# Kernel tuning notes

Hardware: AMD Instinct MI355X
Metric: run time of the kernel (lower is better)

## Reference

```python
import jax, jax.numpy as jnp
import numpy as np

E = 65536
MUL0, MUL1 = 32, 16              # multiplicities of 0e and 1o in irreps_in1/out
FC_IN, FC_HID = 64, 64
WNUMEL = MUL0*MUL0 + MUL1*MUL0 + MUL0*MUL1 + MUL1*MUL1  # 2304
SILU_NORM = 1.6790                # e3nn normalize2mom constant for silu
ISQRT3 = float(1.0 / np.sqrt(3.0))  # w3j entries for l<=1 paths


def setup_inputs() -> dict:
    key = jax.random.key(0)
    k1, k2, k3, k4, k5 = jax.random.split(key, 5)
    return {
        "fea_in1": jax.random.normal(k1, (E, MUL0 + 3 * MUL1), jnp.float32),
        "fea_in2": jax.random.normal(k2, (E, 4), jnp.float32),
        "fea_weight": jax.random.normal(k3, (E, FC_IN), jnp.float32),
        "W1": jax.random.normal(k4, (FC_IN, FC_HID), jnp.float32),
        "W2": jax.random.normal(k5, (FC_HID, WNUMEL), jnp.float32),
    }


def reference(fea_in1, fea_in2, fea_weight, W1, W2):
    # --- e3nn FullyConnectedNet: variance-preserving linear + normalized silu ---
    h = SILU_NORM * jax.nn.silu(fea_weight @ (W1 / np.sqrt(FC_IN)))   # [E, FC_HID]
    w = h @ (W2 / np.sqrt(FC_HID))                                    # [E, WNUMEL]

    # --- split generated per-edge weights into the 4 uvw paths ---
    s0 = MUL0 * MUL0
    s1 = s0 + MUL1 * MUL0
    s2 = s1 + MUL0 * MUL1
    w00 = w[:, :s0].reshape(E, MUL0, MUL0)     # 0e x 0e -> 0e
    w110 = w[:, s0:s1].reshape(E, MUL1, MUL0)  # 1o x 1o -> 0e
    w011 = w[:, s1:s2].reshape(E, MUL0, MUL1)  # 0e x 1o -> 1o
    w101 = w[:, s2:].reshape(E, MUL1, MUL1)    # 1o x 0e -> 1o

    # --- split irrep blocks ---
    x1_0 = fea_in1[:, :MUL0]                       # [E, 32]
    x1_1 = fea_in1[:, MUL0:].reshape(E, MUL1, 3)   # [E, 16, 3]
    x2_0 = fea_in2[:, 0]                           # [E]
    x2_1 = fea_in2[:, 1:4]                         # [E, 3]

    # path weights: sqrt(ir_out.dim / (mul_in1*mul_in2 * n_paths_to_output))
    pw00 = float(np.sqrt(1.0 / (MUL0 * 2)))
    pw110 = float(np.sqrt(1.0 / (MUL1 * 2)))
    pw011 = float(np.sqrt(3.0 / (MUL0 * 2)))
    pw101 = float(np.sqrt(3.0 / (MUL1 * 2)))

    # CG contractions (w3j(0,0,0)=1, w3j(1,1,0)=delta/sqrt3, w3j(0,1,1)=w3j(1,0,1)=delta/sqrt3)
    out0 = pw00 * jnp.einsum('eu,e,euw->ew', x1_0, x2_0, w00) \
         + (pw110 * ISQRT3) * jnp.einsum('eui,ei,euw->ew', x1_1, x2_1, w110)   # [E, 32]
    out1 = (pw011 * ISQRT3) * jnp.einsum('eu,ek,euw->ewk', x1_0, x2_1, w011) \
         + (pw101 * ISQRT3) * jnp.einsum('eui,e,euw->ewi', x1_1, x2_0, w101)   # [E, 16, 3]

    return jnp.concatenate([out0, out1.reshape(E, 3 * MUL1)], axis=1)          # [E, 80]
```

## Files before the change

kernel.cpp:

```cpp
#include <hip/hip_runtime.h>
#include <hip/hip_bf16.h>

typedef __attribute__((ext_vector_type(8)))  __bf16 bf16x8;
typedef __attribute__((ext_vector_type(16))) float  f32x16;

#define N_TILES   72
#define W2F_ELEMS (72*4*64*8)
#define W1F_ELEMS (2*4*64*8)

__global__ __launch_bounds__(256) void equiconv_prep(const float* __restrict__ W1,
                                                     const float* __restrict__ W2,
                                                     __bf16* __restrict__ W1F,
                                                     __bf16* __restrict__ W2F) {
    int idx = blockIdx.x * 256 + threadIdx.x;
    if (idx < W2F_ELEMS) {
        int j  = idx & 7;
        int ln = (idx >> 3) & 63;
        int ks = (idx >> 9) & 3;
        int t  = idx >> 11;
        int m  = 32 * t + (ln & 31);
        int c  = ks * 16 + 8 * (ln >> 5) + j;
        W2F[idx] = (__bf16)(W2[c * 2304 + m] * 0.125f);
    } else {
        int i2 = idx - W2F_ELEMS;
        if (i2 < W1F_ELEMS) {
            int j  = i2 & 7;
            int ln = (i2 >> 3) & 63;
            int ks = (i2 >> 9) & 3;
            int mt = i2 >> 11;
            int c  = 32 * mt + (ln & 31);
            int in = ks * 16 + 8 * (ln >> 5) + j;
            W1F[i2] = (__bf16)(W1[in * 64 + c] * 0.125f);
        }
    }
}

#define X10f(u, el)    smemf[(u)*128 + (el)]
#define CB1f(u, el)    smemf[4096 + (u)*128 + (el)]
#define X11f(k, u, el) smemf[6144 + ((k)*16 + (u))*128 + (el)]
#define F2f(el, j)     smemf[12288 + (el)*4 + (j)]

__global__ __launch_bounds__(256) void equiconv_main(const float* __restrict__ fea_in1,
                                                     const float* __restrict__ fea_in2,
                                                     const float* __restrict__ fea_w,
                                                     const __bf16* __restrict__ W2F,
                                                     const __bf16* __restrict__ W1F,
                                                     float* __restrict__ out) {
    __shared__ __align__(16) float smemf[16896];
    __bf16* HT = (__bf16*)(smemf + 12800);

    const int tid  = threadIdx.x;
    const int lane = tid & 63;
    const int wv   = tid >> 6;
    const int l31  = lane & 31;
    const int hi   = lane >> 5;
    const int eBlk = blockIdx.x * 128;
    const int eLoc = wv * 32 + l31;
    const int sw   = (eLoc & 7) << 3;

    for (int i = tid; i < 128 * 80; i += 256) {
        float v = fea_in1[(size_t)eBlk * 80 + i];
        int el = i / 80;
        int j  = i - el * 80;
        if (j < 32) {
            X10f(j, el) = v;
        } else {
            int jj = j - 32;
            int u  = jj / 3;
            int k  = jj - u * 3;
            X11f(k, u, el) = v;
        }
    }
    for (int i = tid; i < 128 * 4; i += 256)
        F2f(i >> 2, i & 3) = fea_in2[(size_t)eBlk * 4 + i];
    __syncthreads();

    const float c110 = 0.10206207261596577f;
    for (int i = tid; i < 16 * 128; i += 256) {
        int u = i >> 7, el = i & 127;
        CB1f(u, el) = c110 * (X11f(0, u, el) * F2f(el, 1) +
                              X11f(1, u, el) * F2f(el, 2) +
                              X11f(2, u, el) * F2f(el, 3));
    }

    const f32x16 Z16 = {0,0,0,0,0,0,0,0,0,0,0,0,0,0,0,0};
    {
        bf16x8 bw[4];
        const float* pw = fea_w + (size_t)(eBlk + eLoc) * 64 + hi * 8;
#pragma unroll
        for (int ks = 0; ks < 4; ++ks) {
            float4 u0 = *(const float4*)(pw + ks * 16);
            float4 u1 = *(const float4*)(pw + ks * 16 + 4);
            bf16x8 b;
            b[0] = (__bf16)u0.x; b[1] = (__bf16)u0.y; b[2] = (__bf16)u0.z; b[3] = (__bf16)u0.w;
            b[4] = (__bf16)u1.x; b[5] = (__bf16)u1.y; b[6] = (__bf16)u1.z; b[7] = (__bf16)u1.w;
            bw[ks] = b;
        }
        f32x16 h0 = Z16, h1 = Z16;
#pragma unroll
        for (int ks = 0; ks < 4; ++ks) {
            bf16x8 a0 = *(const bf16x8*)(W1F + (size_t)((0 * 4 + ks) * 64 + lane) * 8);
            h0 = __builtin_amdgcn_mfma_f32_32x32x16_bf16(a0, bw[ks], h0, 0, 0, 0);
            bf16x8 a1 = *(const bf16x8*)(W1F + (size_t)((1 * 4 + ks) * 64 + lane) * 8);
            h1 = __builtin_amdgcn_mfma_f32_32x32x16_bf16(a1, bw[ks], h1, 0, 0, 0);
        }
#pragma unroll
        for (int r = 0; r < 16; ++r) {
            int rv = (r & 3) + 8 * (r >> 2) + 4 * hi;
            float x0 = h0[r];
            HT[eLoc * 64 + (rv ^ sw)]        = (__bf16)(1.679f * x0 / (1.f + expf(-x0)));
            float x1 = h1[r];
            HT[eLoc * 64 + ((32 + rv) ^ sw)] = (__bf16)(1.679f * x1 / (1.f + expf(-x1)));
        }
    }
    __syncthreads();

    const float x20  = F2f(eLoc, 0);
    const float x21a = F2f(eLoc, 1), x21b = F2f(eLoc, 2), x21c = F2f(eLoc, 3);
    const float sA0  = 0.125f * x20;
    const float s101 = 0.17677669529663687f * x20;

    bf16x8 hfr[4];
#pragma unroll
    for (int ks = 0; ks < 4; ++ks)
        hfr[ks] = *(const bf16x8*)&HT[eLoc * 64 + ((ks * 16 + 8 * hi) ^ sw)];

    float acc0[16];
    float t011[8];
    float t101[3][8];
#pragma unroll
    for (int r = 0; r < 16; ++r) acc0[r] = 0.f;
#pragma unroll
    for (int s = 0; s < 8; ++s) { t011[s] = 0.f; t101[0][s] = 0.f; t101[1][s] = 0.f; t101[2][s] = 0.f; }

    const __bf16* const pW2l = W2F + (size_t)lane * 8;

#define LOADA(dst, T) {                                                   \
        dst[0] = *(const bf16x8*)(pW2l + (size_t)((T) * 4 + 0) * 512);    \
        dst[1] = *(const bf16x8*)(pW2l + (size_t)((T) * 4 + 1) * 512);    \
        dst[2] = *(const bf16x8*)(pW2l + (size_t)((T) * 4 + 2) * 512);    \
        dst[3] = *(const bf16x8*)(pW2l + (size_t)((T) * 4 + 3) * 512); }

#define MFMA_T(Cv, Af) {                                                          \
        Cv = __builtin_amdgcn_mfma_f32_32x32x16_bf16(Af[0], hfr[0], Z16, 0,0,0);  \
        Cv = __builtin_amdgcn_mfma_f32_32x32x16_bf16(Af[1], hfr[1], Cv,  0,0,0);  \
        Cv = __builtin_amdgcn_mfma_f32_32x32x16_bf16(Af[2], hfr[2], Cv,  0,0,0);  \
        Cv = __builtin_amdgcn_mfma_f32_32x32x16_bf16(Af[3], hfr[3], Cv,  0,0,0); }

#define EPI_W00(TT) { float cf = sA0 * X10f((TT), eLoc);                          \
        _Pragma("unroll") for (int r = 0; r < 16; ++r) acc0[r] += cf * Cv[r]; }
#define EPI_W110(TT) { float cf = CB1f((TT) - 32, eLoc);                          \
        _Pragma("unroll") for (int r = 0; r < 16; ++r) acc0[r] += cf * Cv[r]; }
#define EPI_W011(TT) { int uu = 2 * ((TT) - 48);                                  \
        float cf0 = X10f(uu, eLoc), cf1 = X10f(uu + 1, eLoc);                     \
        _Pragma("unroll") for (int r = 0; r < 16; ++r)                            \
            t011[r & 7] += (r >= 8 ? cf1 : cf0) * Cv[r]; }
#define EPI_W101(TT) { int uu = 2 * ((TT) - 64);                                  \
        float d00 = X11f(0, uu, eLoc), d01 = X11f(1, uu, eLoc), d02 = X11f(2, uu, eLoc);          \
        float d10 = X11f(0, uu + 1, eLoc), d11 = X11f(1, uu + 1, eLoc), d12 = X11f(2, uu + 1, eLoc); \
        _Pragma("unroll") for (int r = 0; r < 16; ++r) {                          \
            int s = r & 7;                                                        \
            t101[0][s] += (r >= 8 ? d10 : d00) * Cv[r];                           \
            t101[1][s] += (r >= 8 ? d11 : d01) * Cv[r];                           \
            t101[2][s] += (r >= 8 ? d12 : d02) * Cv[r]; } }

#define RUN_PHASE(BASE, NT, NEXTT, LAST, EPI)                                     \
    _Pragma("unroll")                                                             \
    for (int t = 0; t < (NT); ++t) {                                              \
        const int cur = (BASE) + t;                                               \
        const int nxt = (t + 1 < (NT)) ? (cur + 1) : (NEXTT);                     \
        f32x16 Cv;                                                                \
        if ((t & 1) == 0) {                                                       \
            if (!(LAST) || (t + 1 < (NT))) LOADA(aQ, nxt);                        \
            MFMA_T(Cv, aP);                                                       \
        } else {                                                                  \
            if (!(LAST) || (t + 1 < (NT))) LOADA(aP, nxt);                        \
            MFMA_T(Cv, aQ);                                                       \
        }                                                                         \
        EPI(cur);                                                                 \
    }

    bf16x8 aP[4], aQ[4];
    LOADA(aP, 0);
    RUN_PHASE(0,  32, 32, false, EPI_W00)
    RUN_PHASE(32, 16, 48, false, EPI_W110)
    RUN_PHASE(48, 16, 64, false, EPI_W011)
    RUN_PHASE(64, 8,  71, true,  EPI_W101)

    __syncthreads();
    float* OST = smemf;
#pragma unroll
    for (int r = 0; r < 16; ++r) {
        int rv = (r & 3) + 8 * (r >> 2) + 4 * hi;
        OST[eLoc * 80 + rv] = acc0[r];
    }
#pragma unroll
    for (int s = 0; s < 8; ++s) {
        int w = (s & 3) + 8 * (s >> 2) + 4 * hi;
        float b011 = 0.125f * t011[s];
        OST[eLoc * 80 + 32 + w * 3 + 0] = x21a * b011 + s101 * t101[0][s];
        OST[eLoc * 80 + 32 + w * 3 + 1] = x21b * b011 + s101 * t101[1][s];
        OST[eLoc * 80 + 32 + w * 3 + 2] = x21c * b011 + s101 * t101[2][s];
    }
    __syncthreads();
    {
        float4* og = (float4*)(out + (size_t)blockIdx.x * 10240);
        const float4* os = (const float4*)smemf;
        for (int i = tid; i < 2560; i += 256) og[i] = os[i];
    }
}

extern "C" void kernel_launch(void* const* d_in, const int* in_sizes, int n_in,
                              void* d_out, int out_size, void* d_ws, size_t ws_size,
                              hipStream_t stream) {
    const float* fea_in1 = (const float*)d_in[0];
    const float* fea_in2 = (const float*)d_in[1];
    const float* fea_w   = (const float*)d_in[2];
    const float* W1      = (const float*)d_in[3];
    const float* W2      = (const float*)d_in[4];
    __bf16* W2F = (__bf16*)d_ws;
    __bf16* W1F = (__bf16*)((char*)d_ws + (size_t)W2F_ELEMS * 2);

    equiconv_prep<<<(W2F_ELEMS + W1F_ELEMS + 255) / 256, 256, 0, stream>>>(W1, W2, W1F, W2F);
    equiconv_main<<<65536 / 128, 256, 0, stream>>>(fea_in1, fea_in2, fea_w, W2F, W1F, (float*)d_out);
}
```

Measured before the change: 133.9 us.

## Stage W2 tiles into LDS via async global_load_lds double buffering

Replaces per-wave register prefetch of W2 fragments with block-cooperative global_load_lds staging into a double-buffered LDS region, adding a block barrier after each of the 72 tiles. It also builds the hidden-activation MFMA operands in registers using packed bf16 conversion and cross-lane shuffles instead of an LDS round trip, switches to fast __expf, and pads the LDS layouts (stride 129/81) to avoid bank conflicts. The goal is to cut redundant per-wave global loads of W2 and LDS traffic, but the per-tile __syncthreads and the scalar un-vectorised output stores may add stalls.

```diff
diff --git a/kernel.cpp b/kernel.cpp
--- a/kernel.cpp
+++ b/kernel.cpp
@@ -7,6 +7,18 @@
 #define N_TILES   72
 #define W2F_ELEMS (72*4*64*8)
 #define W1F_ELEMS (2*4*64*8)
+
+__device__ __forceinline__ void gload_lds16(const void* g, void* l) {
+    __builtin_amdgcn_global_load_lds(
+        (const __attribute__((address_space(1))) unsigned int*)g,
+        (__attribute__((address_space(3))) unsigned int*)l, 16, 0, 0);
+}
+
+__device__ __forceinline__ unsigned pk_bf16(float a, float b) {
+    unsigned r;
+    asm("v_cvt_pk_bf16_f32 %0, %1, %2" : "=v"(r) : "v"(a), "v"(b));
+    return r;
+}
 
 __global__ __launch_bounds__(256) void equiconv_prep(const float* __restrict__ W1,
                                                      const float* __restrict__ W2,
@@ -35,10 +47,11 @@
     }
 }
 
-#define X10f(u, el)    smemf[(u)*128 + (el)]
-#define CB1f(u, el)    smemf[4096 + (u)*128 + (el)]
-#define X11f(k, u, el) smemf[6144 + ((k)*16 + (u))*128 + (el)]
-#define F2f(el, j)     smemf[12288 + (el)*4 + (j)]
+#define X10f(u, el)    smemf[(u)*129 + (el)]
+#define CB1f(u, el)    smemf[4128 + (u)*129 + (el)]
+#define X11f(k, u, el) smemf[6192 + ((u)*3 + (k))*129 + (el)]
+#define F2f(el, j)     smemf[12384 + (el)*4 + (j)]
+#define ASTG_BASE 12896
 
 __global__ __launch_bounds__(256) void equiconv_main(const float* __restrict__ fea_in1,
                                                      const float* __restrict__ fea_in2,
@@ -46,8 +59,7 @@
                                                      const __bf16* __restrict__ W2F,
                                                      const __bf16* __restrict__ W1F,
                                                      float* __restrict__ out) {
-    __shared__ __align__(16) float smemf[16896];
-    __bf16* HT = (__bf16*)(smemf + 12800);
+    __shared__ __align__(16) float smemf[14944];
 
     const int tid  = threadIdx.x;
     const int lane = tid & 63;
@@ -56,7 +68,6 @@
     const int hi   = lane >> 5;
     const int eBlk = blockIdx.x * 128;
     const int eLoc = wv * 32 + l31;
-    const int sw   = (eLoc & 7) << 3;
 
     for (int i = tid; i < 128 * 80; i += 256) {
         float v = fea_in1[(size_t)eBlk * 80 + i];
@@ -84,6 +95,7 @@
     }
 
     const f32x16 Z16 = {0,0,0,0,0,0,0,0,0,0,0,0,0,0,0,0};
+    bf16x8 hfr0, hfr1, hfr2, hfr3;
     {
         bf16x8 bw[4];
         const float* pw = fea_w + (size_t)(eBlk + eLoc) * 64 + hi * 8;
@@ -104,27 +116,46 @@
             bf16x8 a1 = *(const bf16x8*)(W1F + (size_t)((1 * 4 + ks) * 64 + lane) * 8);
             h1 = __builtin_amdgcn_mfma_f32_32x32x16_bf16(a1, bw[ks], h1, 0, 0, 0);
         }
+        float sv[32];
 #pragma unroll
         for (int r = 0; r < 16; ++r) {
-            int rv = (r & 3) + 8 * (r >> 2) + 4 * hi;
             float x0 = h0[r];
-            HT[eLoc * 64 + (rv ^ sw)]        = (__bf16)(1.679f * x0 / (1.f + expf(-x0)));
+            sv[r]      = 1.679f * x0 / (1.f + __expf(-x0));
             float x1 = h1[r];
-            HT[eLoc * 64 + ((32 + rv) ^ sw)] = (__bf16)(1.679f * x1 / (1.f + expf(-x1)));
-        }
-    }
-    __syncthreads();
+            sv[16 + r] = 1.679f * x1 / (1.f + __expf(-x1));
+        }
+        uint4 fr[4];
+#pragma unroll
+        for (int ks = 0; ks < 4; ++ks) {
+            const int vb = 8 * ks;
+            float oa = hi ? sv[vb + 4] : sv[vb + 0];
+            float ob = hi ? sv[vb + 5] : sv[vb + 1];
+            float oc = hi ? sv[vb + 6] : sv[vb + 2];
+            float od = hi ? sv[vb + 7] : sv[vb + 3];
+            float sa = hi ? sv[vb + 0] : sv[vb + 4];
+            float sb = hi ? sv[vb + 1] : sv[vb + 5];
+            float sc = hi ? sv[vb + 2] : sv[vb + 6];
+            float sd = hi ? sv[vb + 3] : sv[vb + 7];
+            unsigned o0 = pk_bf16(oa, ob), o1 = pk_bf16(oc, od);
+            unsigned s0 = pk_bf16(sa, sb), s1 = pk_bf16(sc, sd);
+            unsigned r0 = (unsigned)__shfl_xor((int)s0, 32, 64);
+            unsigned r1 = (unsigned)__shfl_xor((int)s1, 32, 64);
+            fr[ks].x = hi ? r0 : o0;
+            fr[ks].y = hi ? r1 : o1;
+            fr[ks].z = hi ? o0 : r0;
+            fr[ks].w = hi ? o1 : r1;
+        }
+        hfr0 = *(bf16x8*)&fr[0];
+        hfr1 = *(bf16x8*)&fr[1];
+        hfr2 = *(bf16x8*)&fr[2];
+        hfr3 = *(bf16x8*)&fr[3];
+    }
 
     const float x20  = F2f(eLoc, 0);
     const float x21a = F2f(eLoc, 1), x21b = F2f(eLoc, 2), x21c = F2f(eLoc, 3);
     const float sA0  = 0.125f * x20;
     const float s101 = 0.17677669529663687f * x20;
 
-    bf16x8 hfr[4];
-#pragma unroll
-    for (int ks = 0; ks < 4; ++ks)
-        hfr[ks] = *(const bf16x8*)&HT[eLoc * 64 + ((ks * 16 + 8 * hi) ^ sw)];
-
     float acc0[16];
     float t011[8];
     float t101[3][8];
@@ -133,19 +164,14 @@
 #pragma unroll
     for (int s = 0; s < 8; ++s) { t011[s] = 0.f; t101[0][s] = 0.f; t101[1][s] = 0.f; t101[2][s] = 0.f; }
 
-    const __bf16* const pW2l = W2F + (size_t)lane * 8;
-
-#define LOADA(dst, T) {                                                   \
-        dst[0] = *(const bf16x8*)(pW2l + (size_t)((T) * 4 + 0) * 512);    \
-        dst[1] = *(const bf16x8*)(pW2l + (size_t)((T) * 4 + 1) * 512);    \
-        dst[2] = *(const bf16x8*)(pW2l + (size_t)((T) * 4 + 2) * 512);    \
-        dst[3] = *(const bf16x8*)(pW2l + (size_t)((T) * 4 + 3) * 512); }
-
-#define MFMA_T(Cv, Af) {                                                          \
-        Cv = __builtin_amdgcn_mfma_f32_32x32x16_bf16(Af[0], hfr[0], Z16, 0,0,0);  \
-        Cv = __builtin_amdgcn_mfma_f32_32x32x16_bf16(Af[1], hfr[1], Cv,  0,0,0);  \
-        Cv = __builtin_amdgcn_mfma_f32_32x32x16_bf16(Af[2], hfr[2], Cv,  0,0,0);  \
-        Cv = __builtin_amdgcn_mfma_f32_32x32x16_bf16(Af[3], hfr[3], Cv,  0,0,0); }
+    const __bf16* ASTG = (const __bf16*)(smemf + ASTG_BASE);
+    char* stgb = (char*)(smemf + ASTG_BASE);
+    const char* w2b = (const char*)W2F;
+
+#define STAGE(T, BUF) {                                                           \
+        const char* _s = w2b + ((size_t)(T) << 12) + wv * 1024 + (lane << 4);     \
+        char* _d = stgb + ((BUF) << 12) + wv * 1024;                              \
+        gload_lds16(_s, _d); }
 
 #define EPI_W00(TT) { float cf = sA0 * X10f((TT), eLoc);                          \
         _Pragma("unroll") for (int r = 0; r < 16; ++r) acc0[r] += cf * Cv[r]; }
@@ -158,55 +184,62 @@
 #define EPI_W101(TT) { int uu = 2 * ((TT) - 64);                                  \
         float d00 = X11f(0, uu, eLoc), d01 = X11f(1, uu, eLoc), d02 = X11f(2, uu, eLoc);          \
         float d10 = X11f(0, uu + 1, eLoc), d11 = X11f(1, uu + 1, eLoc), d12 = X11f(2, uu + 1, eLoc); \
-        _Pragma("unroll") for (int r = 0; r < 16; ++r) {                          \
-            int s = r & 7;                                                        \
+        _Pragma("unroll") for (int r = 0; r < 16; ++r) { int s = r & 7;           \
             t101[0][s] += (r >= 8 ? d10 : d00) * Cv[r];                           \
             t101[1][s] += (r >= 8 ? d11 : d01) * Cv[r];                           \
             t101[2][s] += (r >= 8 ? d12 : d02) * Cv[r]; } }
 
-#define RUN_PHASE(BASE, NT, NEXTT, LAST, EPI)                                     \
-    _Pragma("unroll")                                                             \
-    for (int t = 0; t < (NT); ++t) {                                              \
-        const int cur = (BASE) + t;                                               \
-        const int nxt = (t + 1 < (NT)) ? (cur + 1) : (NEXTT);                     \
+#define TILE_STEP(T, EPI) {                                                       \
+        if ((T) + 1 < N_TILES) STAGE((T) + 1, bufx ^ 1);                          \
+        const __bf16* tb = ASTG + (bufx << 11) + (lane << 3);                     \
+        bf16x8 a0 = *(const bf16x8*)(tb);                                         \
+        bf16x8 a1 = *(const bf16x8*)(tb + 512);                                   \
+        bf16x8 a2 = *(const bf16x8*)(tb + 1024);                                  \
+        bf16x8 a3 = *(const bf16x8*)(tb + 1536);                                  \
         f32x16 Cv;                                                                \
-        if ((t & 1) == 0) {                                                       \
-            if (!(LAST) || (t + 1 < (NT))) LOADA(aQ, nxt);                        \
-            MFMA_T(Cv, aP);                                                       \
-        } else {                                                                  \
-            if (!(LAST) || (t + 1 < (NT))) LOADA(aP, nxt);                        \
-            MFMA_T(Cv, aQ);                                                       \
-        }                                                                         \
-        EPI(cur);                                                                 \
-    }
-
-    bf16x8 aP[4], aQ[4];
-    LOADA(aP, 0);
-    RUN_PHASE(0,  32, 32, false, EPI_W00)
-    RUN_PHASE(32, 16, 48, false, EPI_W110)
-    RUN_PHASE(48, 16, 64, false, EPI_W011)
-    RUN_PHASE(64, 8,  71, true,  EPI_W101)
-
+        Cv = __builtin_amdgcn_mfma_f32_32x32x16_bf16(a0, hfr0, Z16, 0, 0, 0);     \
+        Cv = __builtin_amdgcn_mfma_f32_32x32x16_bf16(a1, hfr1, Cv, 0, 0, 0);      \
+        Cv = __builtin_amdgcn_mfma_f32_32x32x16_bf16(a2, hfr2, Cv, 0, 0, 0);      \
+        Cv = __builtin_amdgcn_mfma_f32_32x32x16_bf16(a3, hfr3, Cv, 0, 0, 0);      \
+        EPI(T);                                                                   \
+        __syncthreads();                                                          \
+        bufx ^= 1; }
+
+    int bufx = 0;
+    STAGE(0, 0);
     __syncthreads();
+
+#pragma unroll 2
+    for (int t = 0; t < 32; ++t) TILE_STEP(t, EPI_W00)
+#pragma unroll 2
+    for (int t = 32; t < 48; ++t) TILE_STEP(t, EPI_W110)
+#pragma unroll 2
+    for (int t = 48; t < 64; ++t) TILE_STEP(t, EPI_W011)
+#pragma unroll 2
+    for (int t = 64; t < 72; ++t) TILE_STEP(t, EPI_W101)
+
     float* OST = smemf;
 #pragma unroll
     for (int r = 0; r < 16; ++r) {
         int rv = (r & 3) + 8 * (r >> 2) + 4 * hi;
-        OST[eLoc * 80 + rv] = acc0[r];
+        OST[eLoc * 81 + rv] = acc0[r];
     }
 #pragma unroll
     for (int s = 0; s < 8; ++s) {
         int w = (s & 3) + 8 * (s >> 2) + 4 * hi;
         float b011 = 0.125f * t011[s];
-        OST[eLoc * 80 + 32 + w * 3 + 0] = x21a * b011 + s101 * t101[0][s];
-        OST[eLoc * 80 + 32 + w * 3 + 1] = x21b * b011 + s101 * t101[1][s];
-        OST[eLoc * 80 + 32 + w * 3 + 2] = x21c * b011 + s101 * t101[2][s];
+        OST[eLoc * 81 + 32 + w * 3 + 0] = x21a * b011 + s101 * t101[0][s];
+        OST[eLoc * 81 + 32 + w * 3 + 1] = x21b * b011 + s101 * t101[1][s];
+        OST[eLoc * 81 + 32 + w * 3 + 2] = x21c * b011 + s101 * t101[2][s];
     }
     __syncthreads();
     {
-        float4* og = (float4*)(out + (size_t)blockIdx.x * 10240);
-        const float4* os = (const float4*)smemf;
-        for (int i = tid; i < 2560; i += 256) og[i] = os[i];
+        float* og = out + (size_t)blockIdx.x * 10240;
+        for (int i = tid; i < 10240; i += 256) {
+            int el = i / 80;
+            int j  = i - el * 80;
+            og[i] = OST[el * 81 + j];
+        }
     }
 }
 
```

Result: faster. 123.8 us (-7.5%).
